# Optimization experiments

Hardware: AMD Instinct MI355X
Metric: run time of the kernel (lower is better)

Reference implementation:

```python
import jax, jax.numpy as jnp
import numpy as np

B = 8192          # batch
S = 86            # countries (tokens)
D = 64            # embed dim
H = 4             # heads
HD = D // H       # head dim = 16
FEAT = 11         # static country feature dim
R = 7             # regions
HIDDEN = 128


def _build_static():
    """Synthetic (86, 11) static country features matching the real layout:
    [0] stability/4, [1] is_battleground, [2:9] region one-hot, [9:11] start influence/3."""
    rng = np.random.default_rng(0)
    static = np.zeros((S, FEAT), np.float32)
    static[:, 0] = rng.integers(1, 5, S) / 4.0
    static[:, 1] = rng.integers(0, 2, S).astype(np.float32)
    region_id = np.arange(S) % R
    static[np.arange(S), 2 + region_id] = 1.0
    static[:, 9] = np.minimum(rng.integers(0, 4, S) / 3.0, 1.0)
    static[:, 10] = np.minimum(rng.integers(0, 4, S) / 3.0, 1.0)
    return jnp.asarray(static)


def setup_inputs() -> dict:
    key = jax.random.key(0)
    ks = jax.random.split(key, 10)
    influence = jax.random.uniform(ks[0], (B, 2 * S), dtype=jnp.float32) * 4.0
    sc = 0.05
    return {
        "influence": influence,
        "country_static": _build_static(),
        "Wc": jax.random.normal(ks[1], (FEAT + 2, D), jnp.float32) * sc,
        "bc": jax.random.normal(ks[2], (D,), jnp.float32) * sc,
        "Wqkv": jax.random.normal(ks[3], (D, 3 * D), jnp.float32) * sc,
        "bqkv": jax.random.normal(ks[4], (3 * D,), jnp.float32) * sc,
        "Wa": jax.random.normal(ks[5], (D, D), jnp.float32) * sc,
        "ba": jax.random.normal(ks[6], (D,), jnp.float32) * sc,
        "Wo": jax.random.normal(ks[7], ((1 + R) * D, HIDDEN), jnp.float32) * sc,
        "bo": jax.random.normal(ks[8], (HIDDEN,), jnp.float32) * sc,
    }


def reference(influence, country_static, Wc, bc, Wqkv, bqkv, Wa, ba, Wo, bo):
    b = influence.shape[0]
    ussr = influence[:, :S] / 10.0
    us = influence[:, S:] / 10.0
    dyn = jnp.stack([ussr, us], axis=-1)                       # (B, S, 2)
    static = jnp.broadcast_to(country_static[None], (b, S, FEAT))
    feats = jnp.concatenate([dyn, static], axis=-1)            # (B, S, 13)
    tokens = jax.nn.relu(feats @ Wc + bc)                      # (B, S, D)

    qkv = tokens @ Wqkv + bqkv                                 # (B, S, 3D)
    q, k, v = jnp.split(qkv, 3, axis=-1)
    q = q.reshape(b, S, H, HD)
    k = k.reshape(b, S, H, HD)
    v = v.reshape(b, S, H, HD)
    scores = jnp.einsum("bqhd,bkhd->bhqk", q, k) / jnp.sqrt(jnp.float32(HD))
    attn = jax.nn.softmax(scores, axis=-1)
    ctx = jnp.einsum("bhqk,bkhd->bqhd", attn, v).reshape(b, S, D)
    attn_out = ctx @ Wa + ba                                   # (B, S, D)

    global_pool = attn_out.mean(axis=1)                        # (B, D)
    # region masked-mean pooling, vectorized over the 7 regions
    maskf = (country_static[:, 2:2 + R] > 0.5).astype(attn_out.dtype).T  # (R, S)
    counts = maskf.sum(axis=1)                                 # (R,)
    pools = jnp.einsum("rs,bsd->brd", maskf, attn_out) / jnp.maximum(counts, 1.0)[None, :, None]

    concat = jnp.concatenate([global_pool[:, None, :], pools], axis=1).reshape(b, (1 + R) * D)
    return jax.nn.relu(concat @ Wo + bo)                       # (B, 128)
```

## Files before the change

kernel.cpp:

```cpp
#include <hip/hip_runtime.h>

#define B_TOT 8192
#define S86   86

using bf16x8 = __attribute__((ext_vector_type(8))) short;
using u16x8  = __attribute__((ext_vector_type(8))) unsigned short;
using f32x4  = __attribute__((ext_vector_type(4))) float;

#define MFMA(a, b, c) __builtin_amdgcn_mfma_f32_16x16x32_bf16((a), (b), (c), 0, 0, 0)

__device__ inline unsigned short f2bf(float f) {
  unsigned int u = __float_as_uint(f);
  u += 0x7fff + ((u >> 16) & 1);
  return (unsigned short)(u >> 16);
}

#define OFF_SP    0
#define OFF_PWM   22016
#define OFF_INVC  25088
#define OFF_WQKV  25120
#define OFF_WA    49696
#define OFF_WO    57888
#define OFF_C     188960

__global__ void prologue(const float* __restrict__ cstat, const float* __restrict__ Wc,
                         const float* __restrict__ bc, const float* __restrict__ Wqkv,
                         const float* __restrict__ Wa, const float* __restrict__ Wo,
                         float* __restrict__ sp, unsigned short* __restrict__ pwm,
                         float* __restrict__ invc,
                         unsigned short* __restrict__ wqkv_t,
                         unsigned short* __restrict__ wa_t,
                         unsigned short* __restrict__ wo_t) {
  const int b = blockIdx.x, tid = threadIdx.x;
  if (b < 32) {
    #pragma unroll
    for (int ii = 0; ii < 8; ++ii) {
      int idx = ii * 256 + tid;
      int kl = idx >> 7, n = idx & 127;
      int k = b * 16 + kl;
      wo_t[n * 512 + k] = f2bf(Wo[k * 128 + n]);
    }
  } else if (b == 32) {
    for (int i = tid; i < S86 * 64; i += 256) {
      int s = i >> 6, d = i & 63;
      float v = bc[d];
      #pragma unroll
      for (int f = 0; f < 11; ++f) v += cstat[s * 11 + f] * Wc[(2 + f) * 64 + d];
      sp[i] = v;
    }
  } else if (b == 33) {
    for (int i = tid; i < 64 * 192; i += 256) {
      int k = i / 192, n = i % 192;
      wqkv_t[n * 64 + k] = f2bf(Wqkv[i]);
    }
  } else if (b == 34) {
    for (int i = tid; i < 64 * 64; i += 256) {
      int k = i >> 6, n = i & 63;
      wa_t[n * 64 + k] = f2bf(Wa[i]);
    }
  } else {
    __shared__ float rcnt[7];
    if (tid < 7) {
      int c = 0;
      for (int s = 0; s < S86; ++s) c += (cstat[s * 11 + 2 + tid] > 0.5f) ? 1 : 0;
      rcnt[tid] = 1.0f / (float)(c < 1 ? 1 : c);
    }
    __syncthreads();
    for (int i = tid; i < 16 * 96; i += 256) {
      int p = i / 96, s = i - p * 96;
      float v = 0.f;
      if (p < 8 && s < S86)
        v = (p == 0) ? 1.f : ((cstat[s * 11 + 1 + p] > 0.5f) ? 1.f : 0.f);
      pwm[i] = f2bf(v);
    }
    if (tid < 8) invc[tid] = (tid == 0) ? (1.0f / 86.0f) : rcnt[tid - 1];
  }
}

__global__ __launch_bounds__(384, 3) void fused(
    const float* __restrict__ influence, const float* __restrict__ Wc,
    const float* __restrict__ sp, const float* __restrict__ bqkv,
    const float* __restrict__ ba, const float* __restrict__ invc,
    const unsigned short* __restrict__ wqkv_t,
    const unsigned short* __restrict__ wa_t,
    const unsigned short* __restrict__ pwm,
    unsigned short* __restrict__ c_ws) {

  __shared__ __attribute__((aligned(16))) unsigned short s_tok[96 * 64];
  __shared__ __attribute__((aligned(16))) unsigned short s_q[96 * 64];
  __shared__ __attribute__((aligned(16))) unsigned short s_k[96 * 64];
  __shared__ __attribute__((aligned(16))) unsigned short s_v[64 * 96];
  __shared__ __attribute__((aligned(16))) unsigned short s_p[6 * 16 * 104];
  __shared__ __attribute__((aligned(16))) unsigned short s_aoT[64 * 96];

  const int b = blockIdx.x, tid = threadIdx.x;
  const int w = tid >> 6, lane = tid & 63;
  const int g = lane >> 4, lm = lane & 15;
  const f32x4 zf4 = {0.f, 0.f, 0.f, 0.f};
  const bf16x8 z8 = {0, 0, 0, 0, 0, 0, 0, 0};

  #pragma unroll
  for (int it = 0; it < 2; ++it) {
    int i = it * 384 + tid;
    int s = i >> 3, d0 = (i & 7) << 3;
    u16x8 o;
    if (s < S86) {
      float iu = influence[b * 172 + s] * 0.1f;
      float iv = influence[b * 172 + 86 + s] * 0.1f;
      #pragma unroll
      for (int jj = 0; jj < 8; ++jj) {
        int d = d0 + jj;
        float v = fmaxf(iu * Wc[d] + iv * Wc[64 + d] + sp[s * 64 + d], 0.f);
        o[jj] = f2bf(v);
      }
    } else {
      o = (u16x8){0, 0, 0, 0, 0, 0, 0, 0};
    }
    *(u16x8*)&s_tok[s * 64 + (d0 ^ ((s & 7) << 3))] = o;
  }
  __syncthreads();

  {
    bf16x8 bf0[2], bf1[2];
    #pragma unroll
    for (int ks = 0; ks < 2; ++ks) {
      int n0 = (2 * w) * 16 + lm, n1 = (2 * w + 1) * 16 + lm;
      bf0[ks] = *(const bf16x8*)&wqkv_t[n0 * 64 + ks * 32 + g * 8];
      bf1[ks] = *(const bf16x8*)&wqkv_t[n1 * 64 + ks * 32 + g * 8];
    }
    f32x4 acc0[6], acc1[6];
    #pragma unroll
    for (int mt = 0; mt < 6; ++mt) { acc0[mt] = zf4; acc1[mt] = zf4; }
    #pragma unroll
    for (int ks = 0; ks < 2; ++ks)
      #pragma unroll
      for (int mt = 0; mt < 6; ++mt) {
        int m = mt * 16 + lm;
        bf16x8 a = *(const bf16x8*)&s_tok[m * 64 + ((ks * 32 + g * 8) ^ ((m & 7) << 3))];
        acc0[mt] = MFMA(a, bf0[ks], acc0[mt]);
        acc1[mt] = MFMA(a, bf1[ks], acc1[mt]);
      }
    #pragma unroll
    for (int j = 0; j < 2; ++j) {
      int n = (2 * w + j) * 16 + lm;
      float bias = bqkv[n];
      #pragma unroll
      for (int mt = 0; mt < 6; ++mt) {
        f32x4 av = j ? acc1[mt] : acc0[mt];
        #pragma unroll
        for (int r = 0; r < 4; ++r) {
          int m = mt * 16 + 4 * g + r;
          float v = av[r] + bias;
          if (w < 2) {
            s_q[m * 64 + (n ^ ((m & 7) << 3))] = f2bf(v * 0.25f);
          } else if (w < 4) {
            int d = n - 64;
            s_k[m * 64 + (d ^ ((m & 7) << 3))] = f2bf(v);
          } else {
            int d = n - 128;
            s_v[d * 96 + m] = f2bf(v);
          }
        }
      }
    }
  }
  __syncthreads();

  unsigned short* pb = &s_p[w * 16 * 104];
  #pragma unroll
  for (int h = 0; h < 4; ++h) {
    int m = 16 * w + lm;
    int koff = h * 16 + (g & 1) * 8;
    bf16x8 a = *(const bf16x8*)&s_q[m * 64 + (koff ^ ((m & 7) << 3))];
    if (g >= 2) a = z8;
    f32x4 sc[6];
    #pragma unroll
    for (int nt = 0; nt < 6; ++nt) {
      int n = nt * 16 + lm;
      bf16x8 bb = *(const bf16x8*)&s_k[n * 64 + (koff ^ ((n & 7) << 3))];
      sc[nt] = MFMA(a, bb, zf4);
    }
    float inv[4];
    #pragma unroll
    for (int r = 0; r < 4; ++r) {
      float e[6], sum = 0.f;
      #pragma unroll
      for (int nt = 0; nt < 6; ++nt) {
        float x = __expf(sc[nt][r]);
        if (nt == 5 && lm >= 6) x = 0.f;
        e[nt] = x; sum += x;
      }
      sum += __shfl_xor(sum, 1);
      sum += __shfl_xor(sum, 2);
      sum += __shfl_xor(sum, 4);
      sum += __shfl_xor(sum, 8);
      inv[r] = __builtin_amdgcn_rcpf(sum);
      int lr = 4 * g + r;
      #pragma unroll
      for (int nt = 0; nt < 6; ++nt)
        pb[lr * 104 + nt * 16 + lm] = f2bf(e[nt]);
    }
    f32x4 ca = zf4;
    #pragma unroll
    for (int ks = 0; ks < 3; ++ks) {
      bf16x8 pa = *(const bf16x8*)&pb[lm * 104 + ks * 32 + g * 8];
      bf16x8 vb = *(const bf16x8*)&s_v[(h * 16 + lm) * 96 + ks * 32 + g * 8];
      ca = MFMA(pa, vb, ca);
    }
    #pragma unroll
    for (int r = 0; r < 4; ++r) {
      int mm = 16 * w + 4 * g + r;
      int d = h * 16 + lm;
      s_tok[mm * 64 + (d ^ ((mm & 7) << 3))] = f2bf(ca[r] * inv[r]);
    }
  }

  {
    int m = 16 * w + lm;
    bf16x8 a0 = *(const bf16x8*)&s_tok[m * 64 + ((g * 8) ^ ((m & 7) << 3))];
    bf16x8 a1 = *(const bf16x8*)&s_tok[m * 64 + ((32 + g * 8) ^ ((m & 7) << 3))];
    f32x4 acc[4];
    #pragma unroll
    for (int nt = 0; nt < 4; ++nt) acc[nt] = zf4;
    #pragma unroll
    for (int nt = 0; nt < 4; ++nt) {
      int n = nt * 16 + lm;
      bf16x8 b0 = *(const bf16x8*)&wa_t[n * 64 + g * 8];
      bf16x8 b1 = *(const bf16x8*)&wa_t[n * 64 + 32 + g * 8];
      acc[nt] = MFMA(a0, b0, acc[nt]);
      acc[nt] = MFMA(a1, b1, acc[nt]);
    }
    #pragma unroll
    for (int nt = 0; nt < 4; ++nt) {
      int n = nt * 16 + lm;
      float bias = ba[n];
      #pragma unroll
      for (int r = 0; r < 4; ++r) {
        int mm = 16 * w + 4 * g + r;
        s_aoT[n * 96 + mm] = f2bf(acc[nt][r] + bias);
      }
    }
  }
  __syncthreads();

  if (w < 4) {
    f32x4 pc = zf4;
    #pragma unroll
    for (int ks = 0; ks < 3; ++ks) {
      bf16x8 pa = *(const bf16x8*)&pwm[lm * 96 + ks * 32 + g * 8];
      bf16x8 ab = *(const bf16x8*)&s_aoT[(w * 16 + lm) * 96 + ks * 32 + g * 8];
      pc = MFMA(pa, ab, pc);
    }
    if (g < 2) {
      #pragma unroll
      for (int r = 0; r < 4; ++r) {
        int p = 4 * g + r;
        c_ws[b * 512 + p * 64 + w * 16 + lm] = f2bf(pc[r] * invc[p]);
      }
    }
  }
}

__global__ __launch_bounds__(256, 4) void final_gemm(
    const unsigned short* __restrict__ c_ws, const unsigned short* __restrict__ wo_t,
    const float* __restrict__ bo, float* __restrict__ out) {
  __shared__ __attribute__((aligned(16))) unsigned short sA[16 * 512];
  const int tid = threadIdx.x, w = tid >> 6, lane = tid & 63;
  const int g = lane >> 4, lm = lane & 15;
  const int rb = blockIdx.x * 16;
  const f32x4 zf4 = {0.f, 0.f, 0.f, 0.f};

  const uint4* c4 = (const uint4*)c_ws;
  #pragma unroll
  for (int ii = 0; ii < 4; ++ii) {
    int i = ii * 256 + tid;
    int m = i >> 6, d0 = (i & 63) << 3;
    uint4 x = c4[(long)(rb + m) * 64 + (d0 >> 3)];
    *(uint4*)&sA[m * 512 + (d0 ^ ((m & 7) << 3))] = x;
  }
  __syncthreads();

  f32x4 acc0 = zf4, acc1 = zf4;
  const int n0 = (2 * w) * 16 + lm, n1 = (2 * w + 1) * 16 + lm;
  #pragma unroll 4
  for (int ks = 0; ks < 16; ++ks) {
    bf16x8 a = *(const bf16x8*)&sA[lm * 512 + ((ks * 32 + g * 8) ^ ((lm & 7) << 3))];
    bf16x8 b0 = *(const bf16x8*)&wo_t[n0 * 512 + ks * 32 + g * 8];
    bf16x8 b1 = *(const bf16x8*)&wo_t[n1 * 512 + ks * 32 + g * 8];
    acc0 = MFMA(a, b0, acc0);
    acc1 = MFMA(a, b1, acc1);
  }
  float bias0 = bo[n0], bias1 = bo[n1];
  #pragma unroll
  for (int r = 0; r < 4; ++r) {
    int mm = rb + 4 * g + r;
    out[mm * 128 + n0] = fmaxf(acc0[r] + bias0, 0.f);
    out[mm * 128 + n1] = fmaxf(acc1[r] + bias1, 0.f);
  }
}

extern "C" void kernel_launch(void* const* d_in, const int* in_sizes, int n_in,
                              void* d_out, int out_size, void* d_ws, size_t ws_size,
                              hipStream_t stream) {
  const float* influence = (const float*)d_in[0];
  const float* cstat     = (const float*)d_in[1];
  const float* Wc        = (const float*)d_in[2];
  const float* bc        = (const float*)d_in[3];
  const float* Wqkv      = (const float*)d_in[4];
  const float* bqkv      = (const float*)d_in[5];
  const float* Wa        = (const float*)d_in[6];
  const float* ba        = (const float*)d_in[7];
  const float* Wo        = (const float*)d_in[8];
  const float* bo        = (const float*)d_in[9];
  float* out = (float*)d_out;
  char* ws = (char*)d_ws;

  float* sp              = (float*)(ws + OFF_SP);
  unsigned short* pwm    = (unsigned short*)(ws + OFF_PWM);
  float* invc            = (float*)(ws + OFF_INVC);
  unsigned short* wqkv_t = (unsigned short*)(ws + OFF_WQKV);
  unsigned short* wa_t   = (unsigned short*)(ws + OFF_WA);
  unsigned short* wo_t   = (unsigned short*)(ws + OFF_WO);
  unsigned short* c_ws   = (unsigned short*)(ws + OFF_C);

  hipLaunchKernelGGL(prologue, dim3(36), dim3(256), 0, stream,
                     cstat, Wc, bc, Wqkv, Wa, Wo, sp, pwm, invc, wqkv_t, wa_t, wo_t);
  hipLaunchKernelGGL(fused, dim3(B_TOT), dim3(384), 0, stream,
                     influence, Wc, sp, bqkv, ba, invc, wqkv_t, wa_t, pwm, c_ws);
  hipLaunchKernelGGL(final_gemm, dim3(512), dim3(256), 0, stream,
                     c_ws, wo_t, bo, out);
}
```

Baseline: 437.5 us.

## Fuse output GEMM into attention kernel and keep softmax probs in registers

Folds the final Wo projection into the per-sample fused kernel, so the intermediate pooled buffer no longer goes through global memory and the third launch is dropped. Attention is recast as K·Qᵀ so the exponentiated scores can be packed to bf16 and exchanged across lanes with shuffles and perms, replacing the LDS round trip for P and for the context tile. LDS is cut by aliasing buffers. The fused output GEMM uses a single real row of a 16-row MFMA tile, which wastes tensor throughput and rereads Wo once per sample instead of once per 16 samples.

```diff
diff --git a/kernel.cpp b/kernel.cpp
--- a/kernel.cpp
+++ b/kernel.cpp
@@ -13,6 +13,28 @@
   unsigned int u = __float_as_uint(f);
   u += 0x7fff + ((u >> 16) & 1);
   return (unsigned short)(u >> 16);
+}
+__device__ inline unsigned int cvtpk(float lo, float hi) {
+  unsigned int r;
+  asm("v_cvt_pk_bf16_f32 %0, %1, %2" : "=v"(r) : "v"(lo), "v"(hi));
+  return r;
+}
+__device__ inline bf16x8 xchg(unsigned p0, unsigned p1, unsigned p2, unsigned p3,
+                              int slo, int shi, unsigned psel) {
+  unsigned l0 = (unsigned)__shfl((int)p0, slo);
+  unsigned l1 = (unsigned)__shfl((int)p1, slo);
+  unsigned l2 = (unsigned)__shfl((int)p2, slo);
+  unsigned l3 = (unsigned)__shfl((int)p3, slo);
+  unsigned h0 = (unsigned)__shfl((int)p0, shi);
+  unsigned h1 = (unsigned)__shfl((int)p1, shi);
+  unsigned h2 = (unsigned)__shfl((int)p2, shi);
+  unsigned h3 = (unsigned)__shfl((int)p3, shi);
+  uint4 u;
+  u.x = __builtin_amdgcn_perm(l1, l0, psel);
+  u.y = __builtin_amdgcn_perm(l3, l2, psel);
+  u.z = __builtin_amdgcn_perm(h1, h0, psel);
+  u.w = __builtin_amdgcn_perm(h3, h2, psel);
+  return __builtin_bit_cast(bf16x8, u);
 }
 
 #define OFF_SP    0
@@ -21,7 +43,6 @@
 #define OFF_WQKV  25120
 #define OFF_WA    49696
 #define OFF_WO    57888
-#define OFF_C     188960
 
 __global__ void prologue(const float* __restrict__ cstat, const float* __restrict__ Wc,
                          const float* __restrict__ bc, const float* __restrict__ Wqkv,
@@ -81,17 +102,22 @@
     const float* __restrict__ influence, const float* __restrict__ Wc,
     const float* __restrict__ sp, const float* __restrict__ bqkv,
     const float* __restrict__ ba, const float* __restrict__ invc,
+    const float* __restrict__ bo,
     const unsigned short* __restrict__ wqkv_t,
     const unsigned short* __restrict__ wa_t,
     const unsigned short* __restrict__ pwm,
-    unsigned short* __restrict__ c_ws) {
-
-  __shared__ __attribute__((aligned(16))) unsigned short s_tok[96 * 64];
-  __shared__ __attribute__((aligned(16))) unsigned short s_q[96 * 64];
-  __shared__ __attribute__((aligned(16))) unsigned short s_k[96 * 64];
-  __shared__ __attribute__((aligned(16))) unsigned short s_v[64 * 96];
-  __shared__ __attribute__((aligned(16))) unsigned short s_p[6 * 16 * 104];
-  __shared__ __attribute__((aligned(16))) unsigned short s_aoT[64 * 96];
+    const unsigned short* __restrict__ wo_t,
+    float* __restrict__ out) {
+
+  __shared__ __attribute__((aligned(16))) unsigned short s_r1[6656];
+  __shared__ __attribute__((aligned(16))) unsigned short s_q[6144];
+  __shared__ __attribute__((aligned(16))) unsigned short s_r2[6144];
+  __shared__ __attribute__((aligned(16))) unsigned short s_v[6656];
+
+  unsigned short* sT  = s_r1;
+  unsigned short* sAO = s_r1;
+  unsigned short* sK  = s_r2;
+  unsigned short* sCC = s_r2;
 
   const int b = blockIdx.x, tid = threadIdx.x;
   const int w = tid >> 6, lane = tid & 63;
@@ -116,186 +142,155 @@
     } else {
       o = (u16x8){0, 0, 0, 0, 0, 0, 0, 0};
     }
-    *(u16x8*)&s_tok[s * 64 + (d0 ^ ((s & 7) << 3))] = o;
-  }
-  __syncthreads();
-
-  {
-    bf16x8 bf0[2], bf1[2];
-    #pragma unroll
-    for (int ks = 0; ks < 2; ++ks) {
-      int n0 = (2 * w) * 16 + lm, n1 = (2 * w + 1) * 16 + lm;
-      bf0[ks] = *(const bf16x8*)&wqkv_t[n0 * 64 + ks * 32 + g * 8];
-      bf1[ks] = *(const bf16x8*)&wqkv_t[n1 * 64 + ks * 32 + g * 8];
-    }
-    f32x4 acc0[6], acc1[6];
-    #pragma unroll
-    for (int mt = 0; mt < 6; ++mt) { acc0[mt] = zf4; acc1[mt] = zf4; }
-    #pragma unroll
-    for (int ks = 0; ks < 2; ++ks)
-      #pragma unroll
-      for (int mt = 0; mt < 6; ++mt) {
-        int m = mt * 16 + lm;
-        bf16x8 a = *(const bf16x8*)&s_tok[m * 64 + ((ks * 32 + g * 8) ^ ((m & 7) << 3))];
-        acc0[mt] = MFMA(a, bf0[ks], acc0[mt]);
-        acc1[mt] = MFMA(a, bf1[ks], acc1[mt]);
-      }
-    #pragma unroll
-    for (int j = 0; j < 2; ++j) {
-      int n = (2 * w + j) * 16 + lm;
-      float bias = bqkv[n];
-      #pragma unroll
-      for (int mt = 0; mt < 6; ++mt) {
-        f32x4 av = j ? acc1[mt] : acc0[mt];
+    *(u16x8*)&sT[s * 64 + (d0 ^ ((s & 7) << 3))] = o;
+  }
+  __syncthreads();
+
+  const float QS = 0.25f;
+  #pragma unroll
+  for (int j = 0; j < 2; ++j) {
+    int n = (2 * w + j) * 16 + lm;
+    bf16x8 bfr0 = *(const bf16x8*)&wqkv_t[n * 64 + 8 * g];
+    bf16x8 bfr1 = *(const bf16x8*)&wqkv_t[n * 64 + 32 + 8 * g];
+    f32x4 acc[6];
+    #pragma unroll
+    for (int mt = 0; mt < 6; ++mt) acc[mt] = zf4;
+    #pragma unroll
+    for (int mt = 0; mt < 6; ++mt) {
+      int m = mt * 16 + lm;
+      bf16x8 a0 = *(const bf16x8*)&sT[m * 64 + ((8 * g) ^ ((m & 7) << 3))];
+      bf16x8 a1 = *(const bf16x8*)&sT[m * 64 + ((32 + 8 * g) ^ ((m & 7) << 3))];
+      acc[mt] = MFMA(a0, bfr0, acc[mt]);
+      acc[mt] = MFMA(a1, bfr1, acc[mt]);
+    }
+    float bias = bqkv[n];
+    #pragma unroll
+    for (int mt = 0; mt < 6; ++mt)
+      #pragma unroll
+      for (int r = 0; r < 4; ++r) {
+        int m = mt * 16 + 4 * g + r;
+        float v = acc[mt][r] + bias;
+        if (w < 2) {
+          s_q[m * 64 + (n ^ ((m & 7) << 3))] = f2bf(v * QS);
+        } else if (w < 4) {
+          int d = n - 64;
+          sK[m * 64 + (d ^ ((m & 7) << 3))] = f2bf(v);
+        } else {
+          int d = n - 128;
+          s_v[d * 104 + m] = f2bf(v);
+        }
+      }
+  }
+  __syncthreads();
+
+  const int qrow = 16 * w + lm;
+  const int sloLane = ((g & 1) << 5) + lm;
+  const int shiLane = sloLane + 16;
+  const unsigned psel = (g >= 2) ? 0x07060302u : 0x05040100u;
+  f32x4 ctxn[4];
+  #pragma unroll
+  for (int h = 0; h < 4; ++h) {
+    const int koff = h * 16 + (g & 1) * 8;
+    bf16x8 qb = *(const bf16x8*)&s_q[qrow * 64 + (koff ^ ((qrow & 7) << 3))];
+    if (g >= 2) qb = z8;
+    f32x4 sc[6];
+    #pragma unroll
+    for (int mt = 0; mt < 6; ++mt) {
+      int kr = mt * 16 + lm;
+      bf16x8 ka = *(const bf16x8*)&sK[kr * 64 + (koff ^ ((kr & 7) << 3))];
+      sc[mt] = MFMA(ka, qb, zf4);
+    }
+    float ssum = 0.f;
+    #pragma unroll
+    for (int mt = 0; mt < 6; ++mt)
+      #pragma unroll
+      for (int r = 0; r < 4; ++r) {
+        float x = __expf(sc[mt][r]);
+        if (mt == 5 && (4 * g + r) >= 6) x = 0.f;
+        sc[mt][r] = x;
+        ssum += x;
+      }
+    ssum += __shfl_xor(ssum, 16);
+    ssum += __shfl_xor(ssum, 32);
+    float inv = 1.0f / ssum;
+    f32x4 ca = zf4;
+    #pragma unroll
+    for (int ks = 0; ks < 3; ++ks) {
+      unsigned p0 = cvtpk(sc[2 * ks][0], sc[2 * ks + 1][0]);
+      unsigned p1 = cvtpk(sc[2 * ks][1], sc[2 * ks + 1][1]);
+      unsigned p2 = cvtpk(sc[2 * ks][2], sc[2 * ks + 1][2]);
+      unsigned p3 = cvtpk(sc[2 * ks][3], sc[2 * ks + 1][3]);
+      bf16x8 vb = xchg(p0, p1, p2, p3, sloLane, shiLane, psel);
+      bf16x8 va = *(const bf16x8*)&s_v[(h * 16 + lm) * 104 + 32 * ks + 8 * g];
+      ca = MFMA(va, vb, ca);
+    }
+    #pragma unroll
+    for (int r = 0; r < 4; ++r) ctxn[h][r] = ca[r] * inv;
+  }
+
+  f32x4 ao[4];
+  #pragma unroll
+  for (int nt = 0; nt < 4; ++nt) ao[nt] = zf4;
+  #pragma unroll
+  for (int ks = 0; ks < 2; ++ks) {
+    unsigned p0 = cvtpk(ctxn[2 * ks][0], ctxn[2 * ks + 1][0]);
+    unsigned p1 = cvtpk(ctxn[2 * ks][1], ctxn[2 * ks + 1][1]);
+    unsigned p2 = cvtpk(ctxn[2 * ks][2], ctxn[2 * ks + 1][2]);
+    unsigned p3 = cvtpk(ctxn[2 * ks][3], ctxn[2 * ks + 1][3]);
+    bf16x8 ab = xchg(p0, p1, p2, p3, sloLane, shiLane, psel);
+    #pragma unroll
+    for (int nt = 0; nt < 4; ++nt) {
+      bf16x8 wf = *(const bf16x8*)&wa_t[(nt * 16 + lm) * 64 + 32 * ks + 8 * g];
+      ao[nt] = MFMA(wf, ab, ao[nt]);
+    }
+  }
+  __syncthreads();
+  #pragma unroll
+  for (int nt = 0; nt < 4; ++nt)
+    #pragma unroll
+    for (int r = 0; r < 4; ++r) {
+      int n = nt * 16 + 4 * g + r;
+      sAO[n * 104 + 16 * w + lm] = f2bf(ao[nt][r] + ba[n]);
+    }
+  __syncthreads();
+
+  if (w < 4) {
+    f32x4 pc = zf4;
+    #pragma unroll
+    for (int ks = 0; ks < 3; ++ks) {
+      bf16x8 pa  = *(const bf16x8*)&pwm[lm * 96 + 32 * ks + 8 * g];
+      bf16x8 ab2 = *(const bf16x8*)&sAO[(16 * w + lm) * 104 + 32 * ks + 8 * g];
+      pc = MFMA(pa, ab2, pc);
+    }
+    if (g < 2) {
+      #pragma unroll
+      for (int r = 0; r < 4; ++r) {
+        int p = 4 * g + r;
+        sCC[p * 64 + 16 * w + lm] = f2bf(pc[r] * invc[p]);
+      }
+    }
+  }
+  __syncthreads();
+
+  #pragma unroll
+  for (int ti = 0; ti < 2; ++ti) {
+    int t = w + 6 * ti;
+    if (t < 8) {
+      f32x4 fa = zf4;
+      #pragma unroll 4
+      for (int ks = 0; ks < 16; ++ks) {
+        bf16x8 cb = *(const bf16x8*)&sCC[32 * ks + 8 * g];
+        bf16x8 wf = *(const bf16x8*)&wo_t[(t * 16 + lm) * 512 + 32 * ks + 8 * g];
+        fa = MFMA(wf, cb, fa);
+      }
+      if (lm == 0) {
         #pragma unroll
         for (int r = 0; r < 4; ++r) {
-          int m = mt * 16 + 4 * g + r;
-          float v = av[r] + bias;
-          if (w < 2) {
-            s_q[m * 64 + (n ^ ((m & 7) << 3))] = f2bf(v * 0.25f);
-          } else if (w < 4) {
-            int d = n - 64;
-            s_k[m * 64 + (d ^ ((m & 7) << 3))] = f2bf(v);
-          } else {
-            int d = n - 128;
-            s_v[d * 96 + m] = f2bf(v);
-          }
+          int n = t * 16 + 4 * g + r;
+          out[(long)b * 128 + n] = fmaxf(fa[r] + bo[n], 0.f);
         }
       }
     }
-  }
-  __syncthreads();
-
-  unsigned short* pb = &s_p[w * 16 * 104];
-  #pragma unroll
-  for (int h = 0; h < 4; ++h) {
-    int m = 16 * w + lm;
-    int koff = h * 16 + (g & 1) * 8;
-    bf16x8 a = *(const bf16x8*)&s_q[m * 64 + (koff ^ ((m & 7) << 3))];
-    if (g >= 2) a = z8;
-    f32x4 sc[6];
-    #pragma unroll
-    for (int nt = 0; nt < 6; ++nt) {
-      int n = nt * 16 + lm;
-      bf16x8 bb = *(const bf16x8*)&s_k[n * 64 + (koff ^ ((n & 7) << 3))];
-      sc[nt] = MFMA(a, bb, zf4);
-    }
-    float inv[4];
-    #pragma unroll
-    for (int r = 0; r < 4; ++r) {
-      float e[6], sum = 0.f;
-      #pragma unroll
-      for (int nt = 0; nt < 6; ++nt) {
-        float x = __expf(sc[nt][r]);
-        if (nt == 5 && lm >= 6) x = 0.f;
-        e[nt] = x; sum += x;
-      }
-      sum += __shfl_xor(sum, 1);
-      sum += __shfl_xor(sum, 2);
-      sum += __shfl_xor(sum, 4);
-      sum += __shfl_xor(sum, 8);
-      inv[r] = __builtin_amdgcn_rcpf(sum);
-      int lr = 4 * g + r;
-      #pragma unroll
-      for (int nt = 0; nt < 6; ++nt)
-        pb[lr * 104 + nt * 16 + lm] = f2bf(e[nt]);
-    }
-    f32x4 ca = zf4;
-    #pragma unroll
-    for (int ks = 0; ks < 3; ++ks) {
-      bf16x8 pa = *(const bf16x8*)&pb[lm * 104 + ks * 32 + g * 8];
-      bf16x8 vb = *(const bf16x8*)&s_v[(h * 16 + lm) * 96 + ks * 32 + g * 8];
-      ca = MFMA(pa, vb, ca);
-    }
-    #pragma unroll
-    for (int r = 0; r < 4; ++r) {
-      int mm = 16 * w + 4 * g + r;
-      int d = h * 16 + lm;
-      s_tok[mm * 64 + (d ^ ((mm & 7) << 3))] = f2bf(ca[r] * inv[r]);
-    }
-  }
-
-  {
-    int m = 16 * w + lm;
-    bf16x8 a0 = *(const bf16x8*)&s_tok[m * 64 + ((g * 8) ^ ((m & 7) << 3))];
-    bf16x8 a1 = *(const bf16x8*)&s_tok[m * 64 + ((32 + g * 8) ^ ((m & 7) << 3))];
-    f32x4 acc[4];
-    #pragma unroll
-    for (int nt = 0; nt < 4; ++nt) acc[nt] = zf4;
-    #pragma unroll
-    for (int nt = 0; nt < 4; ++nt) {
-      int n = nt * 16 + lm;
-      bf16x8 b0 = *(const bf16x8*)&wa_t[n * 64 + g * 8];
-      bf16x8 b1 = *(const bf16x8*)&wa_t[n * 64 + 32 + g * 8];
-      acc[nt] = MFMA(a0, b0, acc[nt]);
-      acc[nt] = MFMA(a1, b1, acc[nt]);
-    }
-    #pragma unroll
-    for (int nt = 0; nt < 4; ++nt) {
-      int n = nt * 16 + lm;
-      float bias = ba[n];
-      #pragma unroll
-      for (int r = 0; r < 4; ++r) {
-        int mm = 16 * w + 4 * g + r;
-        s_aoT[n * 96 + mm] = f2bf(acc[nt][r] + bias);
-      }
-    }
-  }
-  __syncthreads();
-
-  if (w < 4) {
-    f32x4 pc = zf4;
-    #pragma unroll
-    for (int ks = 0; ks < 3; ++ks) {
-      bf16x8 pa = *(const bf16x8*)&pwm[lm * 96 + ks * 32 + g * 8];
-      bf16x8 ab = *(const bf16x8*)&s_aoT[(w * 16 + lm) * 96 + ks * 32 + g * 8];
-      pc = MFMA(pa, ab, pc);
-    }
-    if (g < 2) {
-      #pragma unroll
-      for (int r = 0; r < 4; ++r) {
-        int p = 4 * g + r;
-        c_ws[b * 512 + p * 64 + w * 16 + lm] = f2bf(pc[r] * invc[p]);
-      }
-    }
-  }
-}
-
-__global__ __launch_bounds__(256, 4) void final_gemm(
-    const unsigned short* __restrict__ c_ws, const unsigned short* __restrict__ wo_t,
-    const float* __restrict__ bo, float* __restrict__ out) {
-  __shared__ __attribute__((aligned(16))) unsigned short sA[16 * 512];
-  const int tid = threadIdx.x, w = tid >> 6, lane = tid & 63;
-  const int g = lane >> 4, lm = lane & 15;
-  const int rb = blockIdx.x * 16;
-  const f32x4 zf4 = {0.f, 0.f, 0.f, 0.f};
-
-  const uint4* c4 = (const uint4*)c_ws;
-  #pragma unroll
-  for (int ii = 0; ii < 4; ++ii) {
-    int i = ii * 256 + tid;
-    int m = i >> 6, d0 = (i & 63) << 3;
-    uint4 x = c4[(long)(rb + m) * 64 + (d0 >> 3)];
-    *(uint4*)&sA[m * 512 + (d0 ^ ((m & 7) << 3))] = x;
-  }
-  __syncthreads();
-
-  f32x4 acc0 = zf4, acc1 = zf4;
-  const int n0 = (2 * w) * 16 + lm, n1 = (2 * w + 1) * 16 + lm;
-  #pragma unroll 4
-  for (int ks = 0; ks < 16; ++ks) {
-    bf16x8 a = *(const bf16x8*)&sA[lm * 512 + ((ks * 32 + g * 8) ^ ((lm & 7) << 3))];
-    bf16x8 b0 = *(const bf16x8*)&wo_t[n0 * 512 + ks * 32 + g * 8];
-    bf16x8 b1 = *(const bf16x8*)&wo_t[n1 * 512 + ks * 32 + g * 8];
-    acc0 = MFMA(a, b0, acc0);
-    acc1 = MFMA(a, b1, acc1);
-  }
-  float bias0 = bo[n0], bias1 = bo[n1];
-  #pragma unroll
-  for (int r = 0; r < 4; ++r) {
-    int mm = rb + 4 * g + r;
-    out[mm * 128 + n0] = fmaxf(acc0[r] + bias0, 0.f);
-    out[mm * 128 + n1] = fmaxf(acc1[r] + bias1, 0.f);
   }
 }
 
@@ -321,12 +316,10 @@
   unsigned short* wqkv_t = (unsigned short*)(ws + OFF_WQKV);
   unsigned short* wa_t   = (unsigned short*)(ws + OFF_WA);
   unsigned short* wo_t   = (unsigned short*)(ws + OFF_WO);
-  unsigned short* c_ws   = (unsigned short*)(ws + OFF_C);
 
   hipLaunchKernelGGL(prologue, dim3(36), dim3(256), 0, stream,
                      cstat, Wc, bc, Wqkv, Wa, Wo, sp, pwm, invc, wqkv_t, wa_t, wo_t);
   hipLaunchKernelGGL(fused, dim3(B_TOT), dim3(384), 0, stream,
-                     influence, Wc, sp, bqkv, ba, invc, wqkv_t, wa_t, pwm, c_ws);
-  hipLaunchKernelGGL(final_gemm, dim3(512), dim3(256), 0, stream,
-                     c_ws, wo_t, bo, out);
-}
+                     influence, Wc, sp, bqkv, ba, invc, bo,
+                     wqkv_t, wa_t, pwm, wo_t, out);
+}
```

Result: faster. 405.3 us (-7.4%).
